# Optimization experiments

Hardware: AMD Instinct MI355X
Metric: run time of the kernel (lower is better)

## Reference

```python
import jax, jax.numpy as jnp
import numpy as np

ATOM_DIM = 34
GAT_DIM = 128
HID_DIM = 256
G_LAYERS = 3
ALPHA = 0.2
NEG_INF = -9e15  # matches torch zero_vec constant


def setup_inputs() -> dict:
    key = jax.random.key(0)
    ks = jax.random.split(key, 10)
    B, N = 64, 512
    compound = jax.random.normal(ks[0], (B, N, ATOM_DIM), dtype=jnp.float32)
    adj = jax.random.randint(ks[1], (B, N, N), 0, 2, dtype=jnp.int32)
    # xavier_uniform gain=1.414 approx: bound = gain*sqrt(6/(fan_in+fan_out))
    def xavier(k, shape, gain=1.414):
        bound = gain * np.sqrt(6.0 / (shape[-2] + shape[-1]))
        return jax.random.uniform(k, shape, jnp.float32, -bound, bound)
    W_stack = xavier(ks[2], (G_LAYERS, ATOM_DIM, GAT_DIM))        # per-layer W
    a_stack = xavier(ks[3], (G_LAYERS, 2 * GAT_DIM, 1))            # per-layer a
    W_out = xavier(ks[4], (G_LAYERS * GAT_DIM, GAT_DIM))           # gat_out.W
    a_out = xavier(ks[5], (2 * GAT_DIM, 1))                        # gat_out.a
    lim = 1.0 / np.sqrt(GAT_DIM)
    Wc = jax.random.uniform(ks[6], (GAT_DIM, HID_DIM), jnp.float32, -lim, lim)  # W_comp weight (in,out)
    bc = jax.random.uniform(ks[7], (HID_DIM,), jnp.float32, -lim, lim)
    return {"compound": compound, "adj": adj, "W_stack": W_stack,
            "a_stack": a_stack, "W_out": W_out, "a_out": a_out,
            "Wc": Wc, "bc": bc}


def _gat_layer(h, adj, W, a, concat):
    # h: [B,N,Fin], adj: [B,N,N], W: [Fin,Fout], a: [2*Fout,1]
    Wh = jnp.einsum('bnf,fg->bng', h, W)                 # [B,N,Fout]
    Fout = W.shape[1]
    # e[b,i,j] = leakyrelu(Wh_i . a1 + Wh_j . a2) == leakyrelu(cat(Wh_i,Wh_j) @ a)
    src = Wh @ a[:Fout, 0]                               # [B,N]
    dst = Wh @ a[Fout:, 0]                               # [B,N]
    e = jax.nn.leaky_relu(src[:, :, None] + dst[:, None, :], ALPHA)  # [B,N,N]
    scores = jnp.where(adj > 0, e, NEG_INF)
    attention = jax.nn.softmax(scores, axis=2)
    h_prime = jnp.einsum('bij,bjf->bif', attention, Wh)  # [B,N,Fout]
    return jax.nn.elu(h_prime) if concat else h_prime


def reference(compound, adj, W_stack, a_stack, W_out, a_out, Wc, bc):
    heads = [_gat_layer(compound, adj, W_stack[l], a_stack[l], concat=True)
             for l in range(G_LAYERS)]
    multi = jnp.concatenate(heads, axis=2)               # [B,N,G_LAYERS*GAT_DIM]
    x = jax.nn.elu(_gat_layer(multi, adj, W_out, a_out, concat=False))
    x = jax.nn.leaky_relu(jnp.einsum('bnf,fh->bnh', x, Wc) + bc, ALPHA)
    return x  # [B,N,HID_DIM]
```

## Files before the change

kernel.cpp:

```cpp
#include <hip/hip_runtime.h>
#include <hip/hip_bf16.h>
#include <math.h>


#define ALPHA 0.2f
#define LOG2E 1.44269504088896f

#if __has_builtin(__builtin_amdgcn_exp2f)
#define EXP2F(x) __builtin_amdgcn_exp2f(x)
#else
extern "C" __device__ float __ocml_exp2_f32(float);
#define EXP2F(x) __ocml_exp2_f32(x)
#endif

typedef __attribute__((ext_vector_type(8))) short s16x8;
typedef __attribute__((ext_vector_type(4))) float f32x4;

__device__ __forceinline__ ushort bf16_rne(float f) {
  union { float f; unsigned u; } v; v.f = f;
  unsigned r = v.u + 0x7FFFu + ((v.u >> 16) & 1u);
  return (ushort)(r >> 16);
}
__device__ __forceinline__ float bf16_tof(ushort h) {
  union { unsigned u; float f; } v; v.u = ((unsigned)h) << 16;
  return v.f;
}
__device__ __forceinline__ void split_store4(
    ushort* __restrict__ ph, ushort* __restrict__ pl,
    float v0, float v1, float v2, float v3) {
  ushort h0 = bf16_rne(v0), h1 = bf16_rne(v1), h2 = bf16_rne(v2), h3 = bf16_rne(v3);
  *(ushort4*)ph = make_ushort4(h0, h1, h2, h3);
  *(ushort4*)pl = make_ushort4(bf16_rne(v0 - bf16_tof(h0)), bf16_rne(v1 - bf16_tof(h1)),
                               bf16_rne(v2 - bf16_tof(h2)), bf16_rne(v3 - bf16_tof(h3)));
}

__device__ __forceinline__ long wht_off(long batch, int c, int j) {
  return batch * 65536 + (long)(c >> 4) * 8192 + (j >> 5) * 512 +
         ((c & 15) << 3) + (((j >> 3) & 3) << 7) + (j & 7);
}

#define WHT_SLOT 8388608L

__global__ __launch_bounds__(256) void wt_prep(
    const float* __restrict__ W, ushort* __restrict__ TH, ushort* __restrict__ TL,
    const int Kd, const int Nd)
{
  const int idx = blockIdx.x * 256 + threadIdx.x;
  if (idx >= Kd * Nd) return;
  const int k = idx / Nd, n = idx % Nd;
  const float v = W[idx];
  const ushort h = bf16_rne(v);
  TH[(long)n * Kd + k] = h;
  TL[(long)n * Kd + k] = bf16_rne(v - bf16_tof(h));
}

__global__ __launch_bounds__(256) void front_union(
    const float* __restrict__ A, const float* __restrict__ Wst,
    const float* __restrict__ ast,
    ushort* __restrict__ whtBase, float* __restrict__ srcB, float* __restrict__ dstB,
    const int* __restrict__ adj, unsigned* __restrict__ mask,
    const float* __restrict__ W_out, ushort* __restrict__ WoT_H, ushort* __restrict__ WoT_L)
{
  __shared__ float AsT[34][36];
  __shared__ float Ws[34][128];
  const int bid = blockIdx.x;
  const int t = threadIdx.x;

  if (bid >= 3072) {
    if (bid < 5120) {
      const int gid = (bid - 3072) * 256 + t;
      const int4* __restrict__ p = (const int4*)(adj + (long)gid * 32);
      unsigned m = 0;
#pragma unroll
      for (int k = 0; k < 8; k++) {
        const int4 v = p[k];
        m |= (v.x > 0 ? 1u : 0u) << (4 * k);
        m |= (v.y > 0 ? 1u : 0u) << (4 * k + 1);
        m |= (v.z > 0 ? 1u : 0u) << (4 * k + 2);
        m |= (v.w > 0 ? 1u : 0u) << (4 * k + 3);
      }
      mask[gid] = m;
    } else {
      const int idx = (bid - 5120) * 256 + t;
      const int k = idx / 128, n = idx % 128;
      const float v = W_out[idx];
      const ushort h = bf16_rne(v);
      WoT_H[(long)n * 384 + k] = h;
      WoT_L[(long)n * 384 + k] = bf16_rne(v - bf16_tof(h));
    }
    return;
  }

  const int l = bid >> 10;
  const float* __restrict__ W = Wst + (long)l * 34 * 128;
  const float* __restrict__ avec = ast + (long)l * 256;
  ushort* __restrict__ whtH = whtBase + (long)l * WHT_SLOT;
  ushort* __restrict__ whtL = whtH + 4194304;
  float* __restrict__ src = srcB + (long)l * 32768;
  float* __restrict__ dst = dstB + (long)l * 32768;
  const long row0 = (long)(bid & 1023) * 32;
  const int cg = t & 31, rg = t >> 5;
  {
    const int r = t >> 3, l8 = t & 7;
#pragma unroll
    for (int q = 0; q < 5; q++) {
      int k = l8 + q * 8;
      if (k < 34) AsT[k][r] = A[(row0 + r) * 34 + k];
    }
  }
  {
    int idx = t;
#pragma unroll
    for (int i = 0; i < 17; i++, idx += 256)
      Ws[idx >> 7][idx & 127] = W[idx];
  }
  __syncthreads();

  float acc[4][4];
#pragma unroll
  for (int r = 0; r < 4; r++)
#pragma unroll
    for (int c = 0; c < 4; c++) acc[r][c] = 0.f;
#pragma unroll 2
  for (int k = 0; k < 34; k++) {
    const float4 wv = *(const float4*)&Ws[k][cg * 4];
    const float4 av = *(const float4*)&AsT[k][rg * 4];
#define GFMA(r, a) \
    acc[r][0] += (a) * wv.x; acc[r][1] += (a) * wv.y; \
    acc[r][2] += (a) * wv.z; acc[r][3] += (a) * wv.w;
    GFMA(0, av.x) GFMA(1, av.y) GFMA(2, av.z) GFMA(3, av.w)
#undef GFMA
  }

  {
    const long batch = row0 >> 9;
    const int j = (int)(row0 & 511) + rg * 4;
#pragma unroll
    for (int cc = 0; cc < 4; cc++) {
      const long o = wht_off(batch, cg * 4 + cc, j);
      split_store4(&whtH[o], &whtL[o], acc[0][cc], acc[1][cc], acc[2][cc], acc[3][cc]);
    }
  }

  const float4 a1 = *(const float4*)&avec[cg * 4];
  const float4 a2 = *(const float4*)&avec[128 + cg * 4];
#pragma unroll
  for (int r = 0; r < 4; r++) {
    float s = acc[r][0]*a1.x + acc[r][1]*a1.y + acc[r][2]*a1.z + acc[r][3]*a1.w;
    float d = acc[r][0]*a2.x + acc[r][1]*a2.y + acc[r][2]*a2.z + acc[r][3]*a2.w;
#pragma unroll
    for (int w = 1; w < 32; w <<= 1) {
      s += __shfl_xor(s, w, 64);
      d += __shfl_xor(d, w, 64);
    }
    if (cg == 0) {
      src[row0 + rg * 4 + r] = s * LOG2E;
      dst[row0 + rg * 4 + r] = d * LOG2E;
    }
  }
}

__global__ __launch_bounds__(256, 4) void fused_attn(
    const unsigned* __restrict__ mask,
    const float* __restrict__ srcB, const float* __restrict__ dstB,
    const ushort* __restrict__ whtBase,
    float* __restrict__ out, const int ostride)
{
  __shared__ ushort As[32][520];
  __shared__ float dstS[512];
  __shared__ float invS[32];
  __shared__ float wredM[4];
  const int t = threadIdx.x;
  const int l = blockIdx.z;
  const float* __restrict__ src = srcB + (long)l * 32768;
  const float* __restrict__ dstv = dstB + (long)l * 32768;
  const ushort* __restrict__ whtH = whtBase + (long)l * WHT_SLOT;
  const ushort* __restrict__ whtL = whtH + 4194304;
  const int ocoff = l * 128;
  const int flat = blockIdx.y * 16 + blockIdx.x;
  const int swz = (flat & 7) * 128 + (flat >> 3);
  const long base = (long)(swz >> 4) * 512;
  const int i0 = (swz & 15) * 32;

  const int wv = t >> 6, lane = t & 63;
  const int m16 = lane & 15, q = lane >> 4;
  const int n0 = wv * 32;
  const ushort* __restrict__ bH = whtH + base * 128 + wv * 16384 + lane * 8;
  const ushort* __restrict__ bL = whtL + base * 128 + wv * 16384 + lane * 8;
  s16x8 pa0H = *(const s16x8*)&bH[0];
  s16x8 pa0L = *(const s16x8*)&bL[0];
  s16x8 pa1H = *(const s16x8*)&bH[8192];
  s16x8 pa1L = *(const s16x8*)&bL[8192];
  s16x8 pb0H = *(const s16x8*)&bH[512];
  s16x8 pb0L = *(const s16x8*)&bL[512];
  s16x8 pb1H = *(const s16x8*)&bH[8192 + 512];
  s16x8 pb1L = *(const s16x8*)&bL[8192 + 512];

  {
    const float d0 = dstv[base + t];
    const float d1 = dstv[base + t + 256];
    dstS[t] = d0;
    dstS[t + 256] = d1;
    float mx = fmaxf(d0, d1);
#pragma unroll
    for (int w = 1; w < 64; w <<= 1) mx = fmaxf(mx, __shfl_xor(mx, w, 64));
    if ((t & 63) == 0) wredM[t >> 6] = mx;
  }
  __syncthreads();
  const float md = fmaxf(fmaxf(wredM[0], wredM[1]), fmaxf(wredM[2], wredM[3]));

  {
    const int r = t >> 3, l8 = t & 7;
    const long i = base + i0 + r;
    const float si = src[i];
    const unsigned* __restrict__ mrow = mask + i * 16;
    unsigned mw[16];
#pragma unroll
    for (int jj = 0; jj < 16; jj++) mw[jj] = mrow[jj];
    const int sh = l8 * 4;
    const float em = si + md;
    const float m = fmaxf(em, ALPHA * em);
    float sum = 0.f;
#pragma unroll
    for (int jj = 0; jj < 16; jj++) {
      const float4 dv = *(const float4*)&dstS[l8 * 4 + jj * 32];
      const unsigned w = mw[jj] >> sh;
      float e0 = si + dv.x, e1 = si + dv.y, e2 = si + dv.z, e3 = si + dv.w;
      e0 = fmaxf(e0, ALPHA * e0) - m; e1 = fmaxf(e1, ALPHA * e1) - m;
      e2 = fmaxf(e2, ALPHA * e2) - m; e3 = fmaxf(e3, ALPHA * e3) - m;
      float p0 = EXP2F(e0), p1 = EXP2F(e1), p2 = EXP2F(e2), p3 = EXP2F(e3);
      p0 = (w & 1u) ? p0 : 0.f;
      p1 = (w & 2u) ? p1 : 0.f;
      p2 = (w & 4u) ? p2 : 0.f;
      p3 = (w & 8u) ? p3 : 0.f;
      sum += (p0 + p1) + (p2 + p3);
      union { __hip_bfloat162 b; unsigned u; } u01, u23;
      u01.b = __float22bfloat162_rn(make_float2(p0, p1));
      u23.b = __float22bfloat162_rn(make_float2(p2, p3));
      *(uint2*)&As[r][l8 * 4 + jj * 32] = make_uint2(u01.u, u23.u);
    }
#pragma unroll
    for (int w = 1; w < 8; w <<= 1) sum += __shfl_xor(sum, w, 64);
    if (l8 == 0) invS[r] = 1.f / sum;
  }
  __syncthreads();

  f32x4 acc00 = {0.f,0.f,0.f,0.f}, acc01 = {0.f,0.f,0.f,0.f};
  f32x4 acc10 = {0.f,0.f,0.f,0.f}, acc11 = {0.f,0.f,0.f,0.f};
#pragma unroll
  for (int kp = 0; kp < 8; kp++) {
    {
      const int k0 = (2 * kp) * 32 + q * 8;
      const s16x8 a0 = *(const s16x8*)&As[m16][k0];
      const s16x8 a1 = *(const s16x8*)&As[16 + m16][k0];
      acc00 = __builtin_amdgcn_mfma_f32_16x16x32_bf16(a0, pa0H, acc00, 0, 0, 0);
      acc01 = __builtin_amdgcn_mfma_f32_16x16x32_bf16(a0, pa1H, acc01, 0, 0, 0);
      acc10 = __builtin_amdgcn_mfma_f32_16x16x32_bf16(a1, pa0H, acc10, 0, 0, 0);
      acc11 = __builtin_amdgcn_mfma_f32_16x16x32_bf16(a1, pa1H, acc11, 0, 0, 0);
      acc00 = __builtin_amdgcn_mfma_f32_16x16x32_bf16(a0, pa0L, acc00, 0, 0, 0);
      acc01 = __builtin_amdgcn_mfma_f32_16x16x32_bf16(a0, pa1L, acc01, 0, 0, 0);
      acc10 = __builtin_amdgcn_mfma_f32_16x16x32_bf16(a1, pa0L, acc10, 0, 0, 0);
      acc11 = __builtin_amdgcn_mfma_f32_16x16x32_bf16(a1, pa1L, acc11, 0, 0, 0);
      if (kp < 7) {
        const int bo = (2 * kp + 2) * 512;
        pa0H = *(const s16x8*)&bH[bo];
        pa0L = *(const s16x8*)&bL[bo];
        pa1H = *(const s16x8*)&bH[8192 + bo];
        pa1L = *(const s16x8*)&bL[8192 + bo];
      }
    }
    {
      const int k0 = (2 * kp + 1) * 32 + q * 8;
      const s16x8 a0 = *(const s16x8*)&As[m16][k0];
      const s16x8 a1 = *(const s16x8*)&As[16 + m16][k0];
      acc00 = __builtin_amdgcn_mfma_f32_16x16x32_bf16(a0, pb0H, acc00, 0, 0, 0);
      acc01 = __builtin_amdgcn_mfma_f32_16x16x32_bf16(a0, pb1H, acc01, 0, 0, 0);
      acc10 = __builtin_amdgcn_mfma_f32_16x16x32_bf16(a1, pb0H, acc10, 0, 0, 0);
      acc11 = __builtin_amdgcn_mfma_f32_16x16x32_bf16(a1, pb1H, acc11, 0, 0, 0);
      acc00 = __builtin_amdgcn_mfma_f32_16x16x32_bf16(a0, pb0L, acc00, 0, 0, 0);
      acc01 = __builtin_amdgcn_mfma_f32_16x16x32_bf16(a0, pb1L, acc01, 0, 0, 0);
      acc10 = __builtin_amdgcn_mfma_f32_16x16x32_bf16(a1, pb0L, acc10, 0, 0, 0);
      acc11 = __builtin_amdgcn_mfma_f32_16x16x32_bf16(a1, pb1L, acc11, 0, 0, 0);
      if (kp < 7) {
        const int bo = (2 * kp + 3) * 512;
        pb0H = *(const s16x8*)&bH[bo];
        pb0L = *(const s16x8*)&bL[bo];
        pb1H = *(const s16x8*)&bH[8192 + bo];
        pb1L = *(const s16x8*)&bL[8192 + bo];
      }
    }
  }
#pragma unroll
  for (int reg = 0; reg < 4; reg++) {
    const int row = q * 4 + reg;
    const float li0 = invS[row], li1 = invS[16 + row];
    float v00 = acc00[reg] * li0, v01 = acc01[reg] * li0;
    float v10 = acc10[reg] * li1, v11 = acc11[reg] * li1;
    v00 = v00 > 0.f ? v00 : __expf(v00) - 1.f;
    v01 = v01 > 0.f ? v01 : __expf(v01) - 1.f;
    v10 = v10 > 0.f ? v10 : __expf(v10) - 1.f;
    v11 = v11 > 0.f ? v11 : __expf(v11) - 1.f;
    float* o0 = out + (base + i0 + row) * (long)ostride + ocoff + n0 + m16;
    float* o1 = out + (base + i0 + 16 + row) * (long)ostride + ocoff + n0 + m16;
    o0[0] = v00; o0[16] = v01;
    o1[0] = v10; o1[16] = v11;
  }
}

template<int K, int KC, int MODE>
__global__ __launch_bounds__(256) void mfma_gemm(
    const float* __restrict__ A,
    const ushort* __restrict__ BTH, const ushort* __restrict__ BTL,
    const float* __restrict__ bias, float* __restrict__ outF,
    ushort* __restrict__ whtH, ushort* __restrict__ whtL,
    const float* __restrict__ avec, float* __restrict__ src, float* __restrict__ dst,
    const int ostride)
{
  constexpr int KP = KC + 8;
  __shared__ ushort AsH[32][KP];
  __shared__ ushort AsL[32][KP];
  __shared__ float sredS[4][32], sredD[4][32];
  const int t = threadIdx.x;
  const long row0 = (long)blockIdx.x * 32;
  const int ncoff = (MODE == 1) ? blockIdx.y * 128 : 0;

  const int wv = t >> 6, lane = t & 63;
  const int m16 = lane & 15, q = lane >> 4;
  const int n0 = wv * 32;
  const ushort* __restrict__ bh0 = BTH + (long)(ncoff + n0 + m16) * K;
  const ushort* __restrict__ bl0 = BTL + (long)(ncoff + n0 + m16) * K;

  f32x4 acc[2][2];
#pragma unroll
  for (int m = 0; m < 2; m++)
#pragma unroll
    for (int n = 0; n < 2; n++) acc[m][n] = (f32x4){0.f, 0.f, 0.f, 0.f};

  for (int kc = 0; kc < K; kc += KC) {
    constexpr int NIT = (32 * KC / 4) / 256;
#pragma unroll
    for (int it = 0; it < NIT; it++) {
      const int idx = t + it * 256;
      const int r = idx / (KC / 4), k4 = idx % (KC / 4);
      const float4 v = *(const float4*)&A[(row0 + r) * (long)K + kc + k4 * 4];
      split_store4(&AsH[r][k4 * 4], &AsL[r][k4 * 4], v.x, v.y, v.z, v.w);
    }
    __syncthreads();
#pragma unroll
    for (int ks = 0; ks < KC / 32; ks++) {
      const int k0 = ks * 32 + q * 8;
      const s16x8 a0H = *(const s16x8*)&AsH[m16][k0];
      const s16x8 a0L = *(const s16x8*)&AsL[m16][k0];
      const s16x8 a1H = *(const s16x8*)&AsH[16 + m16][k0];
      const s16x8 a1L = *(const s16x8*)&AsL[16 + m16][k0];
      const int kg = kc + k0;
      const s16x8 b0H = *(const s16x8*)&bh0[kg];
      const s16x8 b0L = *(const s16x8*)&bl0[kg];
      const s16x8 b1H = *(const s16x8*)&bh0[16 * K + kg];
      const s16x8 b1L = *(const s16x8*)&bl0[16 * K + kg];
      acc[0][0] = __builtin_amdgcn_mfma_f32_16x16x32_bf16(a0H, b0H, acc[0][0], 0, 0, 0);
      acc[0][1] = __builtin_amdgcn_mfma_f32_16x16x32_bf16(a0H, b1H, acc[0][1], 0, 0, 0);
      acc[1][0] = __builtin_amdgcn_mfma_f32_16x16x32_bf16(a1H, b0H, acc[1][0], 0, 0, 0);
      acc[1][1] = __builtin_amdgcn_mfma_f32_16x16x32_bf16(a1H, b1H, acc[1][1], 0, 0, 0);
      acc[0][0] = __builtin_amdgcn_mfma_f32_16x16x32_bf16(a0L, b0H, acc[0][0], 0, 0, 0);
      acc[0][1] = __builtin_amdgcn_mfma_f32_16x16x32_bf16(a0L, b1H, acc[0][1], 0, 0, 0);
      acc[1][0] = __builtin_amdgcn_mfma_f32_16x16x32_bf16(a1L, b0H, acc[1][0], 0, 0, 0);
      acc[1][1] = __builtin_amdgcn_mfma_f32_16x16x32_bf16(a1L, b1H, acc[1][1], 0, 0, 0);
      acc[0][0] = __builtin_amdgcn_mfma_f32_16x16x32_bf16(a0H, b0L, acc[0][0], 0, 0, 0);
      acc[0][1] = __builtin_amdgcn_mfma_f32_16x16x32_bf16(a0H, b1L, acc[0][1], 0, 0, 0);
      acc[1][0] = __builtin_amdgcn_mfma_f32_16x16x32_bf16(a1H, b0L, acc[1][0], 0, 0, 0);
      acc[1][1] = __builtin_amdgcn_mfma_f32_16x16x32_bf16(a1H, b1L, acc[1][1], 0, 0, 0);
    }
    __syncthreads();
  }

  if (MODE == 0) {
    const long batch = row0 >> 9;
    const int iloc = (int)(row0 & 511);
#pragma unroll
    for (int m = 0; m < 2; m++)
#pragma unroll
      for (int n = 0; n < 2; n++) {
        const int c = n0 + n * 16 + m16;
        const int j = iloc + m * 16 + q * 4;
        const long o = wht_off(batch, c, j);
        const f32x4 v = acc[m][n];
        split_store4(&whtH[o], &whtL[o], v[0], v[1], v[2], v[3]);
      }
    const float a10 = avec[n0 + m16], a11 = avec[n0 + 16 + m16];
    const float a20 = avec[128 + n0 + m16], a21 = avec[128 + n0 + 16 + m16];
#pragma unroll
    for (int m = 0; m < 2; m++) {
#pragma unroll
      for (int reg = 0; reg < 4; reg++) {
        float s = acc[m][0][reg] * a10 + acc[m][1][reg] * a11;
        float d = acc[m][0][reg] * a20 + acc[m][1][reg] * a21;
#pragma unroll
        for (int w = 1; w < 16; w <<= 1) {
          s += __shfl_xor(s, w, 64);
          d += __shfl_xor(d, w, 64);
        }
        if (m16 == 0) {
          const int row = m * 16 + q * 4 + reg;
          sredS[wv][row] = s;
          sredD[wv][row] = d;
        }
      }
    }
    __syncthreads();
    if (t < 32) {
      const float s = sredS[0][t] + sredS[1][t] + sredS[2][t] + sredS[3][t];
      const float d = sredD[0][t] + sredD[1][t] + sredD[2][t] + sredD[3][t];
      src[row0 + t] = s * LOG2E;
      dst[row0 + t] = d * LOG2E;
    }
  } else {
#pragma unroll
    for (int m = 0; m < 2; m++)
#pragma unroll
      for (int n = 0; n < 2; n++) {
        const int c = ncoff + n0 + n * 16 + m16;
        const float bv = bias[c];
#pragma unroll
        for (int reg = 0; reg < 4; reg++) {
          float v = acc[m][n][reg] + bv;
          v = fmaxf(v, ALPHA * v);
          outF[(row0 + m * 16 + q * 4 + reg) * (long)ostride + c] = v;
        }
      }
  }
}

extern "C" void kernel_launch(void* const* d_in, const int* in_sizes, int n_in,
                              void* d_out, int out_size, void* d_ws, size_t ws_size,
                              hipStream_t stream) {
  const float* compound = (const float*)d_in[0];
  const int*   adj      = (const int*)d_in[1];
  const float* W_stack  = (const float*)d_in[2];
  const float* a_stack  = (const float*)d_in[3];
  const float* W_out    = (const float*)d_in[4];
  const float* a_out    = (const float*)d_in[5];
  const float* Wc       = (const float*)d_in[6];
  const float* bc       = (const float*)d_in[7];
  float* out = (float*)d_out;

  ushort* wht_all = (ushort*)d_ws;
  float* f     = (float*)d_ws;
  float* multi = f + 12582912;
  float* x     = multi;
  ushort* WcT_H = (ushort*)(multi + 5000000);
  ushort* WcT_L = WcT_H + 32768;

  unsigned* mask = (unsigned*)d_out;
  float* doutF = (float*)d_out;
  float* srcB = doutF + 524288;
  float* dstB = srcB + 4 * 32768;
  ushort* WoT_H = (ushort*)(dstB + 4 * 32768);
  ushort* WoT_L = WoT_H + 98304;
  float* src3 = srcB + 3 * 32768;
  float* dst3 = dstB + 3 * 32768;

  front_union<<<5312, 256, 0, stream>>>(
      compound, W_stack, a_stack, wht_all, srcB, dstB,
      adj, mask, W_out, WoT_H, WoT_L);
  fused_attn<<<dim3(16, 64, 3), 256, 0, stream>>>(
      mask, srcB, dstB, wht_all, multi, 384);
  mfma_gemm<384, 192, 0><<<1024, 256, 0, stream>>>(
      multi, WoT_H, WoT_L, nullptr, nullptr, wht_all, wht_all + 4194304,
      a_out, src3, dst3, 0);
  fused_attn<<<dim3(16, 64, 1), 256, 0, stream>>>(
      mask, src3, dst3, wht_all, x, 128);
  wt_prep<<<128, 256, 0, stream>>>(Wc, WcT_H, WcT_L, 128, 256);
  mfma_gemm<128, 128, 1><<<dim3(1024, 2), 256, 0, stream>>>(
      x, WcT_H, WcT_L, bc, out, nullptr, nullptr, nullptr, nullptr, nullptr, 256);
}
```

Before: 257.5 us.

## Pre-swizzle weights into MFMA fragment order and XOR-swizzle attention LDS tiles

Transposed weight copies are now written in the MFMA B-fragment layout, so the GEMM kernel loads each lane's 8 bf16 values from one contiguous 16-byte location instead of strided rows. In the attention kernel each thread now handles a contiguous 64-column span of the probability row, reading one uint2 of mask words instead of sixteen scattered words. The dst vector in shared memory is padded and the probability tile uses an XOR swizzle on both the store and the MFMA A-operand loads, to reduce LDS bank conflicts. This adds index arithmetic and relies on the writer and reader swizzles matching exactly.

```diff
diff --git a/kernel.cpp b/kernel.cpp
--- a/kernel.cpp
+++ b/kernel.cpp
@@ -36,6 +36,11 @@
 
 __device__ __forceinline__ long wht_off(long batch, int c, int j) {
   return batch * 65536 + (long)(c >> 4) * 8192 + (j >> 5) * 512 +
+         ((c & 15) << 3) + (((j >> 3) & 3) << 7) + (j & 7);
+}
+
+__device__ __forceinline__ long w_frag_off(int c, int j, int Kd) {
+  return (long)(c >> 4) * (Kd * 16) + (j >> 5) * 512 +
          ((c & 15) << 3) + (((j >> 3) & 3) << 7) + (j & 7);
 }
 
@@ -50,8 +55,9 @@
   const int k = idx / Nd, n = idx % Nd;
   const float v = W[idx];
   const ushort h = bf16_rne(v);
-  TH[(long)n * Kd + k] = h;
-  TL[(long)n * Kd + k] = bf16_rne(v - bf16_tof(h));
+  const long o = w_frag_off(n, k, Kd);
+  TH[o] = h;
+  TL[o] = bf16_rne(v - bf16_tof(h));
 }
 
 __global__ __launch_bounds__(256) void front_union(
@@ -85,8 +91,9 @@
       const int k = idx / 128, n = idx % 128;
       const float v = W_out[idx];
       const ushort h = bf16_rne(v);
-      WoT_H[(long)n * 384 + k] = h;
-      WoT_L[(long)n * 384 + k] = bf16_rne(v - bf16_tof(h));
+      const long o = w_frag_off(n, k, 384);
+      WoT_H[o] = h;
+      WoT_L[o] = bf16_rne(v - bf16_tof(h));
     }
     return;
   }
@@ -167,7 +174,7 @@
     float* __restrict__ out, const int ostride)
 {
   __shared__ ushort As[32][520];
-  __shared__ float dstS[512];
+  __shared__ float dstS[544];
   __shared__ float invS[32];
   __shared__ float wredM[4];
   const int t = threadIdx.x;
@@ -199,8 +206,9 @@
   {
     const float d0 = dstv[base + t];
     const float d1 = dstv[base + t + 256];
-    dstS[t] = d0;
-    dstS[t + 256] = d1;
+    dstS[t + (t >> 6) * 4] = d0;
+    const int t2 = t + 256;
+    dstS[t2 + (t2 >> 6) * 4] = d1;
     float mx = fmaxf(d0, d1);
 #pragma unroll
     for (int w = 1; w < 64; w <<= 1) mx = fmaxf(mx, __shfl_xor(mx, w, 64));
@@ -213,18 +221,17 @@
     const int r = t >> 3, l8 = t & 7;
     const long i = base + i0 + r;
     const float si = src[i];
-    const unsigned* __restrict__ mrow = mask + i * 16;
-    unsigned mw[16];
-#pragma unroll
-    for (int jj = 0; jj < 16; jj++) mw[jj] = mrow[jj];
-    const int sh = l8 * 4;
+    const uint2 mw2 = *(const uint2*)(mask + i * 16 + 2 * l8);
     const float em = si + md;
     const float m = fmaxf(em, ALPHA * em);
+    const float* __restrict__ dp = &dstS[l8 * 68];
+    const int jb = l8 * 64;
+    const int xs = l8 << 3;
     float sum = 0.f;
 #pragma unroll
-    for (int jj = 0; jj < 16; jj++) {
-      const float4 dv = *(const float4*)&dstS[l8 * 4 + jj * 32];
-      const unsigned w = mw[jj] >> sh;
+    for (int g = 0; g < 16; g++) {
+      const float4 dv = *(const float4*)&dp[g * 4];
+      const unsigned w = ((g & 8) ? mw2.y : mw2.x) >> ((g & 7) * 4);
       float e0 = si + dv.x, e1 = si + dv.y, e2 = si + dv.z, e3 = si + dv.w;
       e0 = fmaxf(e0, ALPHA * e0) - m; e1 = fmaxf(e1, ALPHA * e1) - m;
       e2 = fmaxf(e2, ALPHA * e2) - m; e3 = fmaxf(e3, ALPHA * e3) - m;
@@ -237,7 +244,7 @@
       union { __hip_bfloat162 b; unsigned u; } u01, u23;
       u01.b = __float22bfloat162_rn(make_float2(p0, p1));
       u23.b = __float22bfloat162_rn(make_float2(p2, p3));
-      *(uint2*)&As[r][l8 * 4 + jj * 32] = make_uint2(u01.u, u23.u);
+      *(uint2*)&As[r][(jb + g * 4) ^ xs] = make_uint2(u01.u, u23.u);
     }
 #pragma unroll
     for (int w = 1; w < 8; w <<= 1) sum += __shfl_xor(sum, w, 64);
@@ -250,7 +257,7 @@
 #pragma unroll
   for (int kp = 0; kp < 8; kp++) {
     {
-      const int k0 = (2 * kp) * 32 + q * 8;
+      const int k0 = ((2 * kp) * 32 + q * 8) ^ (kp << 3);
       const s16x8 a0 = *(const s16x8*)&As[m16][k0];
       const s16x8 a1 = *(const s16x8*)&As[16 + m16][k0];
       acc00 = __builtin_amdgcn_mfma_f32_16x16x32_bf16(a0, pa0H, acc00, 0, 0, 0);
@@ -270,7 +277,7 @@
       }
     }
     {
-      const int k0 = (2 * kp + 1) * 32 + q * 8;
+      const int k0 = ((2 * kp + 1) * 32 + q * 8) ^ (kp << 3);
       const s16x8 a0 = *(const s16x8*)&As[m16][k0];
       const s16x8 a1 = *(const s16x8*)&As[16 + m16][k0];
       acc00 = __builtin_amdgcn_mfma_f32_16x16x32_bf16(a0, pb0H, acc00, 0, 0, 0);
@@ -327,8 +334,8 @@
   const int wv = t >> 6, lane = t & 63;
   const int m16 = lane & 15, q = lane >> 4;
   const int n0 = wv * 32;
-  const ushort* __restrict__ bh0 = BTH + (long)(ncoff + n0 + m16) * K;
-  const ushort* __restrict__ bl0 = BTL + (long)(ncoff + n0 + m16) * K;
+  const ushort* __restrict__ bh0 = BTH + (long)((ncoff + n0) >> 4) * (K * 16) + lane * 8;
+  const ushort* __restrict__ bl0 = BTL + (long)((ncoff + n0) >> 4) * (K * 16) + lane * 8;
 
   f32x4 acc[2][2];
 #pragma unroll
@@ -353,11 +360,11 @@
       const s16x8 a0L = *(const s16x8*)&AsL[m16][k0];
       const s16x8 a1H = *(const s16x8*)&AsH[16 + m16][k0];
       const s16x8 a1L = *(const s16x8*)&AsL[16 + m16][k0];
-      const int kg = kc + k0;
-      const s16x8 b0H = *(const s16x8*)&bh0[kg];
-      const s16x8 b0L = *(const s16x8*)&bl0[kg];
-      const s16x8 b1H = *(const s16x8*)&bh0[16 * K + kg];
-      const s16x8 b1L = *(const s16x8*)&bl0[16 * K + kg];
+      const int bo = ((kc >> 5) + ks) * 512;
+      const s16x8 b0H = *(const s16x8*)&bh0[bo];
+      const s16x8 b0L = *(const s16x8*)&bl0[bo];
+      const s16x8 b1H = *(const s16x8*)&bh0[K * 16 + bo];
+      const s16x8 b1L = *(const s16x8*)&bl0[K * 16 + bo];
       acc[0][0] = __builtin_amdgcn_mfma_f32_16x16x32_bf16(a0H, b0H, acc[0][0], 0, 0, 0);
       acc[0][1] = __builtin_amdgcn_mfma_f32_16x16x32_bf16(a0H, b1H, acc[0][1], 0, 0, 0);
       acc[1][0] = __builtin_amdgcn_mfma_f32_16x16x32_bf16(a1H, b0H, acc[1][0], 0, 0, 0);
```

Measured after the change: 241.5 us. 6.2% less time.
